# Kernel optimization log

Hardware: AMD Instinct MI355X
Metric: run time of the kernel (lower is better)

Reference implementation:

```python
import jax, jax.numpy as jnp
import numpy as np

N_CLASSES = 128
NAN_TO = 0.0


def setup_inputs() -> dict:
    key = jax.random.key(0)
    k1, k2 = jax.random.split(key)
    B, n = 500000, N_CLASSES
    y_hat = jax.random.normal(k1, (B, n), dtype=jnp.float32)
    y = jax.random.uniform(k2, (B, n), dtype=jnp.float32)
    return {"y_hat": y_hat, "y": y}


def reference(y_hat, y):
    # class id per sample (argmax over class dim)
    y_cls = jnp.argmax(y, axis=1)  # [B] int
    # per-sample loss (loss_fn with reduction='none'): soft-target cross entropy
    loss = -jnp.sum(y * jax.nn.log_softmax(y_hat, axis=-1), axis=1)  # [B]
    # per-class mean via a single-pass segment reduce (replaces the O(n*B) mask loop)
    seg_sum = jax.ops.segment_sum(loss, y_cls, num_segments=N_CLASSES)
    counts = jax.ops.segment_sum(jnp.ones_like(loss), y_cls, num_segments=N_CLASSES)
    # mean over an empty class would be NaN in torch; replaced by nan_to
    out = jnp.where(counts > 0, seg_sum / jnp.maximum(counts, 1.0), NAN_TO)
    return out
```

## Files before the change

kernel.cpp:

```cpp
#include <hip/hip_runtime.h>

#define N_CLASSES 128

__global__ __launch_bounds__(256) void class_loss_kernel(
    const float* __restrict__ y_hat,
    const float* __restrict__ y,
    float* __restrict__ ws,
    int B)
{
    __shared__ float s_sum[N_CLASSES];
    __shared__ float s_cnt[N_CLASSES];
    const int tid = threadIdx.x;
    for (int i = tid; i < N_CLASSES; i += blockDim.x) { s_sum[i] = 0.f; s_cnt[i] = 0.f; }
    __syncthreads();

    const int lane    = tid & 31;
    const int group   = (blockIdx.x * blockDim.x + tid) >> 5;
    const int ngroups = (gridDim.x * blockDim.x) >> 5;

    for (int row = group; row < B; row += ngroups) {
        const float4 h4 = ((const float4*)(y_hat + (size_t)row * N_CLASSES))[lane];
        const float4 t4 = ((const float4*)(y     + (size_t)row * N_CLASSES))[lane];

        float m = fmaxf(fmaxf(h4.x, h4.y), fmaxf(h4.z, h4.w));
        #pragma unroll
        for (int o = 16; o >= 1; o >>= 1) m = fmaxf(m, __shfl_xor(m, o, 32));

        float s   = __expf(h4.x - m) + __expf(h4.y - m) + __expf(h4.z - m) + __expf(h4.w - m);
        float dot = t4.x * h4.x + t4.y * h4.y + t4.z * h4.z + t4.w * h4.w;
        float sy  = t4.x + t4.y + t4.z + t4.w;

        float bv = t4.x; int bi = lane * 4;
        if (t4.y > bv) { bv = t4.y; bi = lane * 4 + 1; }
        if (t4.z > bv) { bv = t4.z; bi = lane * 4 + 2; }
        if (t4.w > bv) { bv = t4.w; bi = lane * 4 + 3; }

        #pragma unroll
        for (int o = 16; o >= 1; o >>= 1) {
            s   += __shfl_xor(s,   o, 32);
            dot += __shfl_xor(dot, o, 32);
            sy  += __shfl_xor(sy,  o, 32);
            float ov = __shfl_xor(bv, o, 32);
            int   oi = __shfl_xor(bi, o, 32);
            if (ov > bv || (ov == bv && oi < bi)) { bv = ov; bi = oi; }
        }

        if (lane == 0) {
            float loss = (m + __logf(s)) * sy - dot;
            atomicAdd(&s_sum[bi], loss);
            atomicAdd(&s_cnt[bi], 1.0f);
        }
    }

    __syncthreads();
    for (int i = tid; i < N_CLASSES; i += blockDim.x) {
        if (s_cnt[i] > 0.f) {
            atomicAdd(&ws[i], s_sum[i]);
            atomicAdd(&ws[N_CLASSES + i], s_cnt[i]);
        }
    }
}

__global__ void finalize_kernel(const float* __restrict__ ws, float* __restrict__ out) {
    const int c = threadIdx.x;
    if (c < N_CLASSES) {
        float cnt = ws[N_CLASSES + c];
        out[c] = (cnt > 0.f) ? ws[c] / cnt : 0.0f;
    }
}

extern "C" void kernel_launch(void* const* d_in, const int* in_sizes, int n_in,
                              void* d_out, int out_size, void* d_ws, size_t ws_size,
                              hipStream_t stream) {
    const float* y_hat = (const float*)d_in[0];
    const float* y     = (const float*)d_in[1];
    float* ws  = (float*)d_ws;
    float* out = (float*)d_out;
    const int B = in_sizes[0] / N_CLASSES;

    hipMemsetAsync(d_ws, 0, 2 * N_CLASSES * sizeof(float), stream);

    const int blocks = 1024;
    class_loss_kernel<<<blocks, 256, 0, stream>>>(y_hat, y, ws, B);
    finalize_kernel<<<1, N_CLASSES, 0, stream>>>(ws, out);
}
```

Baseline: 491.1 us.

## Process each row with 16 lanes, two float4s each, and simplify argmax reduction

Each row is now handled by 16 lanes instead of 32, with every lane loading two float4 chunks of logits and targets. This halves the shuffle-reduction depth per row and doubles the loads in flight per lane. The argmax is split into a max reduction followed by a min-index reduction over matching positions, which replaces the paired value/index shuffles. The grid is doubled to 2048 blocks and launch bounds request 8 blocks per CU, which raises occupancy pressure and the number of shared-atomic flushes per block.

```diff
diff --git a/kernel.cpp b/kernel.cpp
--- a/kernel.cpp
+++ b/kernel.cpp
@@ -2,7 +2,7 @@
 
 #define N_CLASSES 128
 
-__global__ __launch_bounds__(256) void class_loss_kernel(
+__global__ __launch_bounds__(256, 8) void class_loss_kernel(
     const float* __restrict__ y_hat,
     const float* __restrict__ y,
     float* __restrict__ ws,
@@ -14,35 +14,53 @@
     for (int i = tid; i < N_CLASSES; i += blockDim.x) { s_sum[i] = 0.f; s_cnt[i] = 0.f; }
     __syncthreads();
 
-    const int lane    = tid & 31;
-    const int group   = (blockIdx.x * blockDim.x + tid) >> 5;
-    const int ngroups = (gridDim.x * blockDim.x) >> 5;
+    const int lane    = tid & 15;
+    const int group   = (blockIdx.x * blockDim.x + tid) >> 4;
+    const int ngroups = (gridDim.x * blockDim.x) >> 4;
+
+    const float4* __restrict__ ph = (const float4*)y_hat;
+    const float4* __restrict__ pt = (const float4*)y;
 
     for (int row = group; row < B; row += ngroups) {
-        const float4 h4 = ((const float4*)(y_hat + (size_t)row * N_CLASSES))[lane];
-        const float4 t4 = ((const float4*)(y     + (size_t)row * N_CLASSES))[lane];
+        const size_t base = (size_t)row * (N_CLASSES / 4);
+        const float4 h0 = ph[base + lane];
+        const float4 h1 = ph[base + lane + 16];
+        const float4 t0 = pt[base + lane];
+        const float4 t1 = pt[base + lane + 16];
 
-        float m = fmaxf(fmaxf(h4.x, h4.y), fmaxf(h4.z, h4.w));
+        float m  = fmaxf(fmaxf(fmaxf(h0.x, h0.y), fmaxf(h0.z, h0.w)),
+                         fmaxf(fmaxf(h1.x, h1.y), fmaxf(h1.z, h1.w)));
+        float bv = fmaxf(fmaxf(fmaxf(t0.x, t0.y), fmaxf(t0.z, t0.w)),
+                         fmaxf(fmaxf(t1.x, t1.y), fmaxf(t1.z, t1.w)));
         #pragma unroll
-        for (int o = 16; o >= 1; o >>= 1) m = fmaxf(m, __shfl_xor(m, o, 32));
+        for (int o = 8; o >= 1; o >>= 1) {
+            m  = fmaxf(m,  __shfl_xor(m,  o));
+            bv = fmaxf(bv, __shfl_xor(bv, o));
+        }
 
-        float s   = __expf(h4.x - m) + __expf(h4.y - m) + __expf(h4.z - m) + __expf(h4.w - m);
-        float dot = t4.x * h4.x + t4.y * h4.y + t4.z * h4.z + t4.w * h4.w;
-        float sy  = t4.x + t4.y + t4.z + t4.w;
+        float s = __expf(h0.x - m) + __expf(h0.y - m) + __expf(h0.z - m) + __expf(h0.w - m)
+                + __expf(h1.x - m) + __expf(h1.y - m) + __expf(h1.z - m) + __expf(h1.w - m);
+        float dot = t0.x * h0.x + t0.y * h0.y + t0.z * h0.z + t0.w * h0.w
+                  + t1.x * h1.x + t1.y * h1.y + t1.z * h1.z + t1.w * h1.w;
+        float sy = (t0.x + t0.y + t0.z + t0.w) + (t1.x + t1.y + t1.z + t1.w);
 
-        float bv = t4.x; int bi = lane * 4;
-        if (t4.y > bv) { bv = t4.y; bi = lane * 4 + 1; }
-        if (t4.z > bv) { bv = t4.z; bi = lane * 4 + 2; }
-        if (t4.w > bv) { bv = t4.w; bi = lane * 4 + 3; }
+        const int e0 = lane * 4, e1 = 64 + lane * 4;
+        int bi = N_CLASSES;
+        bi = (t1.w == bv) ? e1 + 3 : bi;
+        bi = (t1.z == bv) ? e1 + 2 : bi;
+        bi = (t1.y == bv) ? e1 + 1 : bi;
+        bi = (t1.x == bv) ? e1     : bi;
+        bi = (t0.w == bv) ? e0 + 3 : bi;
+        bi = (t0.z == bv) ? e0 + 2 : bi;
+        bi = (t0.y == bv) ? e0 + 1 : bi;
+        bi = (t0.x == bv) ? e0     : bi;
 
         #pragma unroll
-        for (int o = 16; o >= 1; o >>= 1) {
-            s   += __shfl_xor(s,   o, 32);
-            dot += __shfl_xor(dot, o, 32);
-            sy  += __shfl_xor(sy,  o, 32);
-            float ov = __shfl_xor(bv, o, 32);
-            int   oi = __shfl_xor(bi, o, 32);
-            if (ov > bv || (ov == bv && oi < bi)) { bv = ov; bi = oi; }
+        for (int o = 8; o >= 1; o >>= 1) {
+            s   += __shfl_xor(s,   o);
+            dot += __shfl_xor(dot, o);
+            sy  += __shfl_xor(sy,  o);
+            bi   = min(bi, __shfl_xor(bi, o));
         }
 
         if (lane == 0) {
@@ -80,7 +98,7 @@
 
     hipMemsetAsync(d_ws, 0, 2 * N_CLASSES * sizeof(float), stream);
 
-    const int blocks = 1024;
+    const int blocks = 2048;
     class_loss_kernel<<<blocks, 256, 0, stream>>>(y_hat, y, ws, B);
     finalize_kernel<<<1, N_CLASSES, 0, stream>>>(ws, out);
 }
```

After: 489.7 us. No clear change (-0.3%).
